# Kernel tuning notes

Hardware: AMD Instinct MI355X
Metric: run time of the kernel (lower is better)

## Reference

```python
import jax, jax.numpy as jnp
import numpy as np

B, S, D = 32, 2048, 1024
TEMP = 9.0  # RelaxedBernoulli temperature (torch.tensor([9]))


def setup_inputs() -> dict:
    key = jax.random.key(0)
    ks = jax.random.split(key, 12)
    sd = 1.0 / np.sqrt(D)
    sd2 = 1.0 / np.sqrt(2 * D)
    return {
        "h_t": jax.random.normal(ks[0], (B, D), jnp.float32),
        "h_s": jax.random.normal(ks[1], (B, S, D), jnp.float32),
        "auxi_hs": jax.random.normal(ks[2], (B, S, D), jnp.float32),
        "noise_u": jax.random.uniform(ks[3], (B, S, 1), jnp.float32),
        # linear_map: Linear(2*dim, 1) with bias
        "Wmap": jax.random.normal(ks[4], (2 * D,), jnp.float32) * sd2,
        "bmap": jax.random.normal(ks[5], (), jnp.float32) * sd2,
        # mlp_h: Linear(dim, dim) + Tanh + Linear(dim, 1)
        "W1": jax.random.normal(ks[6], (D, D), jnp.float32) * sd,
        "b1": jax.random.normal(ks[7], (D,), jnp.float32) * sd,
        "W2": jax.random.normal(ks[8], (D,), jnp.float32) * sd,
        "b2": jax.random.normal(ks[9], (), jnp.float32) * sd,
        # linear_out: Linear(2*dim, dim, bias=False) (attn_type='dot')
        "Wout": jax.random.normal(ks[10], (D, 2 * D), jnp.float32) * sd2,
    }


def reference(h_t, h_s, auxi_hs, noise_u, Wmap, bmap, W1, b1, W2, b2, Wout):
    # h_t: (B, D) one-step query; h_s, auxi_hs: (B, S, D)
    d = h_s.shape[-1]
    # linear_map(concat(auxi_hs, H_t)) without materializing the (B,S,2D) concat
    Wm_a, Wm_t = Wmap[:d], Wmap[d:]
    logits_p = jnp.einsum('bsd,d->bs', auxi_hs, Wm_a) + (h_t @ Wm_t)[:, None] + bmap  # (B,S)
    logits_p = logits_p[..., None]  # (B,S,1); note logit(sigmoid(x)) == x
    # RelaxedBernoulli(temp=9, probs=sigmoid(logits_p)).sample() with explicit uniform noise
    eps = 1e-7
    u = jnp.clip(noise_u, eps, 1.0 - eps)
    logistic = jnp.log(u) - jnp.log1p(-u)  # (B,S,1)
    G = jax.nn.sigmoid((logits_p + logistic) / TEMP)  # (B,S,1)
    # mlp_h(h_s): Linear -> tanh -> Linear
    e = jnp.einsum('bsd,d->bs', jnp.tanh(jnp.einsum('bsd,ed->bse', h_s, W1) + b1), W2) + b2
    e = e[..., None]  # (B,S,1)
    # custom softmax: max over dim 0 (batch!), exp, gate
    v = jnp.max(e, axis=0, keepdims=True)  # (1,S,1)
    scores = jnp.exp(e - v) * G  # (B,S,1)
    align = scores[..., 0] / jnp.sum(scores[..., 0], axis=1, keepdims=True)  # (B,S)
    c = jnp.einsum('bs,bsd->bd', align, h_s)  # (B,D)
    attn_h = jnp.tanh(jnp.concatenate([c, h_t], axis=-1) @ Wout.T)  # (B,D)
    return attn_h, align
```

## Files before the change

### kernel.cpp

```cpp
#include <hip/hip_runtime.h>
#include <hip/hip_bf16.h>
#include <math.h>

#define B_ 32
#define S_ 2048
#define D_ 1024
#define TEMP_ 9.0f

typedef __attribute__((ext_vector_type(8))) short short8;
typedef __attribute__((ext_vector_type(4))) float f32x4;
typedef __attribute__((ext_vector_type(4))) unsigned short ushort4v;

__device__ __forceinline__ unsigned short f2b(float f) {
  union { float f; unsigned int u; } v; v.f = f;
  unsigned int r = v.u;
  r += 0x7fffu + ((r >> 16) & 1u);
  return (unsigned short)(r >> 16);
}
__device__ __forceinline__ float b2f(unsigned short b) {
  union { float f; unsigned int u; } v; v.u = ((unsigned int)b) << 16;
  return v.f;
}
__device__ __forceinline__ float tanh_fast(float x) {
  float ez = __expf(2.f * x);
  return 1.f - __fdividef(2.f, ez + 1.f);
}

#define GLOAD_LDS16(g, l) \
  __builtin_amdgcn_global_load_lds((const __attribute__((address_space(1))) void*)(g), \
                                   (__attribute__((address_space(3))) void*)(l), 16, 0, 0)

__global__ void k_conv(const float* __restrict__ src, unsigned short* __restrict__ dst, int n8) {
  int i = blockIdx.x * 256 + threadIdx.x;
  if (i >= n8) return;
  const float4* g = reinterpret_cast<const float4*>(src) + (size_t)i * 2;
  float4 x0 = g[0], x1 = g[1];
  uint4 w;
  w.x = f2b(x0.x) | ((unsigned)f2b(x0.y) << 16);
  w.y = f2b(x0.z) | ((unsigned)f2b(x0.w) << 16);
  w.z = f2b(x1.x) | ((unsigned)f2b(x1.y) << 16);
  w.w = f2b(x1.z) | ((unsigned)f2b(x1.w) << 16);
  reinterpret_cast<uint4*>(dst)[i] = w;
}

__global__ void k0_tdot(const float* __restrict__ h_t, const float* __restrict__ Wmap,
                        const float* __restrict__ bmap, float* __restrict__ tdot) {
  int b = blockIdx.x;
  int t = threadIdx.x;
  float p = 0.f;
  for (int k = t; k < D_; k += 256) p += h_t[b*D_ + k] * Wmap[D_ + k];
  __shared__ float red[256];
  red[t] = p; __syncthreads();
  for (int off = 128; off > 0; off >>= 1) { if (t < off) red[t] += red[t+off]; __syncthreads(); }
  if (t == 0) tdot[b] = red[0] + bmap[0];
}

__global__ void k1_gate(const float* __restrict__ aux, const float* __restrict__ Wmap,
                        const float* __restrict__ noise, const float* __restrict__ tdot,
                        float* __restrict__ Gout) {
  int w = (blockIdx.x * 256 + threadIdx.x) >> 6;
  int lane = threadIdx.x & 63;
  const float4* arow = reinterpret_cast<const float4*>(aux + (size_t)w * D_);
  const float4* wrow = reinterpret_cast<const float4*>(Wmap);
  float p = 0.f;
  for (int it = 0; it < 4; ++it) {
    float4 a = arow[it*64 + lane];
    float4 m = wrow[it*64 + lane];
    p += a.x*m.x + a.y*m.y + a.z*m.z + a.w*m.w;
  }
  for (int msk = 32; msk > 0; msk >>= 1) p += __shfl_xor(p, msk);
  if (lane == 0) {
    int b = w >> 11;
    float logits = p + tdot[b];
    float u = noise[w];
    u = fminf(fmaxf(u, 1e-7f), 1.f - 1e-7f);
    float logistic = logf(u) - log1pf(-u);
    float x = (logits + logistic) / TEMP_;
    Gout[w] = 1.f / (1.f + expf(-x));
  }
}

#define BK3 32
#define NT3 (D_ / BK3)
#define A_BYTES 8192
#define B_BYTES 16384
#define BUF_BYTES 24576
#define NBUF 3

extern __shared__ unsigned short lds2[];

__global__ __launch_bounds__(256, 2) void k2_pipe(
    const unsigned short* __restrict__ Ag, const unsigned short* __restrict__ Bg,
    const float* __restrict__ b1, const float* __restrict__ W2,
    float* __restrict__ e_buf) {
  int hw = blockIdx.x;
  int xcd = hw & 7;
  int sub = hw >> 3;
  int cc  = sub & 3;
  int rc  = xcd + 8 * (sub >> 2);
  int rowBase = rc * 128;
  int colBase = cc * 256;

  int t = threadIdx.x;
  int lane = t & 63;
  int wc = t >> 6;
  int kslot = lane >> 4;

  int aOff[8], bOff[4];
#pragma unroll
  for (int m = 0; m < 8; ++m) {
    int ra = m * 16 + (lane & 15);
    aOff[m] = ra * 64 + ((kslot ^ ((ra >> 1) & 3)) << 4);
  }
#pragma unroll
  for (int n = 0; n < 4; ++n) {
    int rb = wc * 64 + n * 16 + (lane & 15);
    bOff[n] = A_BYTES + rb * 64 + ((kslot ^ ((rb >> 1) & 3)) << 4);
  }

  const unsigned short* gA[2];
  const unsigned short* gB[4];
  int dstA[2], dstB[4];
#pragma unroll
  for (int i = 0; i < 2; ++i) {
    int c = i * 256 + t;
    int r = c >> 2;
    int clog = (c & 3) ^ ((r >> 1) & 3);
    gA[i] = Ag + (size_t)(rowBase + r) * D_ + clog * 8;
    dstA[i] = c * 16;
  }
#pragma unroll
  for (int i = 0; i < 4; ++i) {
    int c = i * 256 + t;
    int r = c >> 2;
    int clog = (c & 3) ^ ((r >> 1) & 3);
    gB[i] = Bg + (size_t)(colBase + r) * D_ + clog * 8;
    dstB[i] = A_BYTES + c * 16;
  }

  f32x4 acc[8][4] = {};

#define STAGE(TT) do {                                                         \
    char* _ba = (char*)lds2 + ((TT) % NBUF) * BUF_BYTES;                       \
    GLOAD_LDS16(gA[0] + (TT) * 32, _ba + dstA[0]);                             \
    GLOAD_LDS16(gA[1] + (TT) * 32, _ba + dstA[1]);                             \
    GLOAD_LDS16(gB[0] + (TT) * 32, _ba + dstB[0]);                             \
    GLOAD_LDS16(gB[1] + (TT) * 32, _ba + dstB[1]);                             \
    GLOAD_LDS16(gB[2] + (TT) * 32, _ba + dstB[2]);                             \
    GLOAD_LDS16(gB[3] + (TT) * 32, _ba + dstB[3]);                             \
  } while (0)

#define K2_TILE(T, VM, DO_STAGE) do {                                          \
    asm volatile("s_waitcnt lgkmcnt(0)\n\ts_waitcnt vmcnt(" #VM ")" ::: "memory"); \
    __builtin_amdgcn_s_barrier();                                              \
    const char* _ab = (const char*)lds2 + ((T) % NBUF) * BUF_BYTES;            \
    short8 af[8], bf[4];                                                       \
    _Pragma("unroll")                                                          \
    for (int n = 0; n < 4; ++n)                                                \
      bf[n] = *reinterpret_cast<const short8*>(_ab + bOff[n]);                 \
    _Pragma("unroll")                                                          \
    for (int m = 0; m < 4; ++m)                                                \
      af[m] = *reinterpret_cast<const short8*>(_ab + aOff[m]);                 \
    if (DO_STAGE) STAGE((T) + 2);                                              \
    __builtin_amdgcn_s_setprio(1);                                             \
    _Pragma("unroll")                                                          \
    for (int m = 0; m < 4; ++m)                                                \
      _Pragma("unroll")                                                        \
      for (int n = 0; n < 4; ++n)                                              \
        acc[m][n] = __builtin_amdgcn_mfma_f32_16x16x32_bf16(af[m], bf[n], acc[m][n], 0, 0, 0); \
    __builtin_amdgcn_s_setprio(0);                                             \
    _Pragma("unroll")                                                          \
    for (int m = 4; m < 8; ++m)                                                \
      af[m] = *reinterpret_cast<const short8*>(_ab + aOff[m]);                 \
    __builtin_amdgcn_s_setprio(1);                                             \
    _Pragma("unroll")                                                          \
    for (int m = 4; m < 8; ++m)                                                \
      _Pragma("unroll")                                                        \
      for (int n = 0; n < 4; ++n)                                              \
        acc[m][n] = __builtin_amdgcn_mfma_f32_16x16x32_bf16(af[m], bf[n], acc[m][n], 0, 0, 0); \
    __builtin_amdgcn_s_setprio(0);                                             \
  } while (0)

  STAGE(0); STAGE(1);
#pragma unroll
  for (int tt = 0; tt < 30; ++tt) K2_TILE(tt, 6, true);
  K2_TILE(30, 6, false);
  K2_TILE(31, 0, false);
#undef K2_TILE
#undef STAGE

  float b1v[4], w2v[4];
#pragma unroll
  for (int n = 0; n < 4; ++n) {
    int col = colBase + wc * 64 + n * 16 + (lane & 15);
    b1v[n] = b1[col];
    w2v[n] = W2[col];
  }
#pragma unroll
  for (int m = 0; m < 8; ++m) {
#pragma unroll
    for (int j = 0; j < 4; ++j) {
      float s = 0.f;
#pragma unroll
      for (int n = 0; n < 4; ++n)
        s += tanh_fast(acc[m][n][j] + b1v[n]) * w2v[n];
      s += __shfl_xor(s, 1);
      s += __shfl_xor(s, 2);
      s += __shfl_xor(s, 4);
      s += __shfl_xor(s, 8);
      if ((lane & 15) == 0) {
        int row = rowBase + m * 16 + ((lane >> 4) << 2) + j;
        atomicAdd(&e_buf[row], s);
      }
    }
  }
}

#define BM 128
#define BN 128
#define BK 64
__global__ __launch_bounds__(256) void k2_egemm_f32(
    const float* __restrict__ h_s, const float* __restrict__ W1,
    const float* __restrict__ b1, const float* __restrict__ W2,
    float* __restrict__ e_buf) {
  __shared__ unsigned short As[BM * BK];
  __shared__ unsigned short Bs[BN * BK];
  int bid = blockIdx.x;
  int colBase = (bid & 7) * BN;
  int rowBase = (bid >> 3) * BM;
  int t = threadIdx.x;
  int lane = t & 63;
  int wave = t >> 6;
  int wr = wave >> 1, wc = wave & 1;
  f32x4 acc[4][4] = {};
  for (int k0 = 0; k0 < D_; k0 += BK) {
    __syncthreads();
    for (int i = 0; i < 4; ++i) {
      int flat = i*256 + t;
      int r = flat >> 3;
      int c8 = flat & 7;
      int byte = (r*128 + c8*16) ^ ((r & 7) << 4);
      {
        const float4* g = reinterpret_cast<const float4*>(h_s + (size_t)(rowBase + r)*D_ + k0 + c8*8);
        float4 x0 = g[0], x1 = g[1];
        uint4 w;
        w.x = f2b(x0.x) | ((unsigned)f2b(x0.y) << 16);
        w.y = f2b(x0.z) | ((unsigned)f2b(x0.w) << 16);
        w.z = f2b(x1.x) | ((unsigned)f2b(x1.y) << 16);
        w.w = f2b(x1.z) | ((unsigned)f2b(x1.w) << 16);
        *reinterpret_cast<uint4*>(reinterpret_cast<char*>(As) + byte) = w;
      }
      {
        const float4* g = reinterpret_cast<const float4*>(W1 + (size_t)(colBase + r)*D_ + k0 + c8*8);
        float4 x0 = g[0], x1 = g[1];
        uint4 w;
        w.x = f2b(x0.x) | ((unsigned)f2b(x0.y) << 16);
        w.y = f2b(x0.z) | ((unsigned)f2b(x0.w) << 16);
        w.z = f2b(x1.x) | ((unsigned)f2b(x1.y) << 16);
        w.w = f2b(x1.z) | ((unsigned)f2b(x1.w) << 16);
        *reinterpret_cast<uint4*>(reinterpret_cast<char*>(Bs) + byte) = w;
      }
    }
    __syncthreads();
    for (int kk = 0; kk < BK; kk += 32) {
      short8 af[4], bf[4];
      int kByte = kk*2 + ((lane >> 4) << 4);
      for (int m = 0; m < 4; ++m) {
        int r = wr*64 + m*16 + (lane & 15);
        int byte = (r*128 + kByte) ^ ((r & 7) << 4);
        af[m] = *reinterpret_cast<const short8*>(reinterpret_cast<const char*>(As) + byte);
      }
      for (int n = 0; n < 4; ++n) {
        int r = wc*64 + n*16 + (lane & 15);
        int byte = (r*128 + kByte) ^ ((r & 7) << 4);
        bf[n] = *reinterpret_cast<const short8*>(reinterpret_cast<const char*>(Bs) + byte);
      }
      for (int m = 0; m < 4; ++m)
        for (int n = 0; n < 4; ++n)
          acc[m][n] = __builtin_amdgcn_mfma_f32_16x16x32_bf16(af[m], bf[n], acc[m][n], 0, 0, 0);
    }
  }
  float b1v[4], w2v[4];
  for (int n = 0; n < 4; ++n) {
    int col = colBase + wc*64 + n*16 + (lane & 15);
    b1v[n] = b1[col];
    w2v[n] = W2[col];
  }
  for (int m = 0; m < 4; ++m) {
    for (int j = 0; j < 4; ++j) {
      float s = 0.f;
      for (int n = 0; n < 4; ++n)
        s += tanhf(acc[m][n][j] + b1v[n]) * w2v[n];
      s += __shfl_xor(s, 1);
      s += __shfl_xor(s, 2);
      s += __shfl_xor(s, 4);
      s += __shfl_xor(s, 8);
      if ((lane & 15) == 0) {
        int row = rowBase + wr*64 + m*16 + ((lane >> 4) << 2) + j;
        atomicAdd(&e_buf[row], s);
      }
    }
  }
}

__global__ void k3a_vmax(const float* __restrict__ e_buf, float* __restrict__ v) {
  int s = blockIdx.x * 256 + threadIdx.x;
  if (s >= S_) return;
  float m = -1e30f;
  for (int b = 0; b < B_; ++b) m = fmaxf(m, e_buf[b*S_ + s]);
  v[s] = m;
}

__global__ void k3b_align(const float* __restrict__ e_buf, const float* __restrict__ v,
                          float* __restrict__ galign) {
  int b = blockIdx.x;
  int t = threadIdx.x;
  __shared__ float sc[S_];
  __shared__ float red[256];
  float p = 0.f;
  for (int s = t; s < S_; s += 256) {
    float x = expf(e_buf[b*S_ + s] - v[s]) * galign[b*S_ + s];
    sc[s] = x;
    p += x;
  }
  red[t] = p; __syncthreads();
  for (int off = 128; off > 0; off >>= 1) { if (t < off) red[t] += red[t+off]; __syncthreads(); }
  float inv = 1.f / red[0];
  for (int s = t; s < S_; s += 256) galign[b*S_ + s] = sc[s] * inv;
}

__global__ void k4_ctx_bf16(const unsigned short* __restrict__ hsb, const float* __restrict__ align,
                            float* __restrict__ c) {
  int bid = blockIdx.x;
  int b = bid >> 6;
  int sBase = (bid & 63) * 32;
  int t = threadIdx.x;
  float4 accv = {0.f, 0.f, 0.f, 0.f};
  for (int si = 0; si < 32; ++si) {
    int s = sBase + si;
    float a = align[b*S_ + s];
    ushort4v hv = *reinterpret_cast<const ushort4v*>(hsb + (size_t)(b*S_ + s)*D_ + t*4);
    accv.x += a*b2f(hv.x); accv.y += a*b2f(hv.y); accv.z += a*b2f(hv.z); accv.w += a*b2f(hv.w);
  }
  atomicAdd(&c[b*D_ + t*4 + 0], accv.x);
  atomicAdd(&c[b*D_ + t*4 + 1], accv.y);
  atomicAdd(&c[b*D_ + t*4 + 2], accv.z);
  atomicAdd(&c[b*D_ + t*4 + 3], accv.w);
}

__global__ void k4_ctx_f32(const float* __restrict__ h_s, const float* __restrict__ align,
                           float* __restrict__ c) {
  int bid = blockIdx.x;
  int b = bid >> 6;
  int sBase = (bid & 63) * 32;
  int t = threadIdx.x;
  float4 accv = {0.f, 0.f, 0.f, 0.f};
  for (int si = 0; si < 32; ++si) {
    int s = sBase + si;
    float a = align[b*S_ + s];
    float4 hv = *reinterpret_cast<const float4*>(h_s + (size_t)(b*S_ + s)*D_ + t*4);
    accv.x += a*hv.x; accv.y += a*hv.y; accv.z += a*hv.z; accv.w += a*hv.w;
  }
  atomicAdd(&c[b*D_ + t*4 + 0], accv.x);
  atomicAdd(&c[b*D_ + t*4 + 1], accv.y);
  atomicAdd(&c[b*D_ + t*4 + 2], accv.z);
  atomicAdd(&c[b*D_ + t*4 + 3], accv.w);
}

__global__ void k5_out(const float* __restrict__ c, const float* __restrict__ h_t,
                       const float* __restrict__ Wout, float* __restrict__ out) {
  int W = (blockIdx.x * 256 + threadIdx.x) >> 6;
  int lane = threadIdx.x & 63;
  int b = W >> 10;
  int o = W & 1023;
  const float* wrow = Wout + (size_t)o * (2 * D_);
  float p = 0.f;
  for (int it = 0; it < 16; ++it) {
    int k = it*64 + lane;
    p += c[b*D_ + k] * wrow[k];
  }
  for (int it = 16; it < 32; ++it) {
    int k = it*64 + lane;
    p += h_t[b*D_ + (k - D_)] * wrow[k];
  }
  for (int m = 32; m > 0; m >>= 1) p += __shfl_xor(p, m);
  if (lane == 0) out[b*D_ + o] = tanhf(p);
}

extern "C" void kernel_launch(void* const* d_in, const int* in_sizes, int n_in,
                              void* d_out, int out_size, void* d_ws, size_t ws_size,
                              hipStream_t stream) {
  const float* h_t   = (const float*)d_in[0];
  const float* h_s   = (const float*)d_in[1];
  const float* aux   = (const float*)d_in[2];
  const float* noise = (const float*)d_in[3];
  const float* Wmap  = (const float*)d_in[4];
  const float* bmap  = (const float*)d_in[5];
  const float* W1    = (const float*)d_in[6];
  const float* b1    = (const float*)d_in[7];
  const float* W2    = (const float*)d_in[8];
  const float* Wout  = (const float*)d_in[10];

  float* out    = (float*)d_out;
  float* galign = out + B_*D_;

  const size_t HS_N   = (size_t)B_*S_*D_;
  const size_t W1_N   = (size_t)D_*D_;
  const size_t needed = HS_N*2 + W1_N*2 + (65536 + 32 + 2048 + 32768) * sizeof(float);

  if (ws_size >= needed) {
    unsigned short* hs_bf = (unsigned short*)d_ws;
    unsigned short* w1_bf = hs_bf + HS_N;
    float* fws   = (float*)(w1_bf + W1_N);
    float* e_buf = fws;
    float* tdot  = fws + 65536;
    float* v     = fws + 65568;
    float* c     = fws + 67616;

    hipMemsetAsync(e_buf, 0, 65536 * sizeof(float), stream);
    hipMemsetAsync(c, 0, 32768 * sizeof(float), stream);

    hipFuncSetAttribute(reinterpret_cast<const void*>(k2_pipe),
                        hipFuncAttributeMaxDynamicSharedMemorySize, NBUF * BUF_BYTES);

    k_conv<<<(int)(HS_N/8/256), 256, 0, stream>>>(h_s, hs_bf, (int)(HS_N/8));
    k_conv<<<(int)(W1_N/8/256), 256, 0, stream>>>(W1, w1_bf, (int)(W1_N/8));
    k0_tdot<<<32, 256, 0, stream>>>(h_t, Wmap, bmap, tdot);
    k1_gate<<<16384, 256, 0, stream>>>(aux, Wmap, noise, tdot, galign);
    k2_pipe<<<2048, 256, NBUF * BUF_BYTES, stream>>>(hs_bf, w1_bf, b1, W2, e_buf);
    k3a_vmax<<<8, 256, 0, stream>>>(e_buf, v);
    k3b_align<<<32, 256, 0, stream>>>(e_buf, v, galign);
    k4_ctx_bf16<<<2048, 256, 0, stream>>>(hs_bf, galign, c);
    k5_out<<<8192, 256, 0, stream>>>(c, h_t, Wout, out);
  } else {
    float* ws    = (float*)d_ws;
    float* e_buf = ws;
    float* tdot  = ws + 65536;
    float* v     = ws + 65568;
    float* c     = ws + 67616;

    hipMemsetAsync(e_buf, 0, 65536 * sizeof(float), stream);
    hipMemsetAsync(c, 0, 32768 * sizeof(float), stream);

    k0_tdot<<<32, 256, 0, stream>>>(h_t, Wmap, bmap, tdot);
    k1_gate<<<16384, 256, 0, stream>>>(aux, Wmap, noise, tdot, galign);
    k2_egemm_f32<<<4096, 256, 0, stream>>>(h_s, W1, b1, W2, e_buf);
    k3a_vmax<<<8, 256, 0, stream>>>(e_buf, v);
    k3b_align<<<32, 256, 0, stream>>>(e_buf, v, galign);
    k4_ctx_f32<<<2048, 256, 0, stream>>>(h_s, galign, c);
    k5_out<<<8192, 256, 0, stream>>>(c, h_t, Wout, out);
  }
}
```

Measured before the change: 357.2 us.

## Pre-pack W1 into MFMA fragment layout and load B operand directly into registers

A new kernel packs W1 into bf16 in MFMA B-fragment order, so each wave can read its B operands straight from global memory into registers, double-buffered across K tiles. Only the A tile now goes through LDS, with a 4-deep ring of 8KB buffers staged three tiles ahead. The aim is to cut LDS traffic, barrier pressure and LDS footprint in the main GEMM. The cost is that B reads no longer share data within a block: each wave issues its own global loads, which makes the loop more exposed to global memory latency.

```diff
diff --git a/kernel.cpp b/kernel.cpp
--- a/kernel.cpp
+++ b/kernel.cpp
@@ -41,6 +41,24 @@
   w.z = f2b(x1.x) | ((unsigned)f2b(x1.y) << 16);
   w.w = f2b(x1.z) | ((unsigned)f2b(x1.w) << 16);
   reinterpret_cast<uint4*>(dst)[i] = w;
+}
+
+__global__ void k_pack_w1(const float* __restrict__ W1, unsigned short* __restrict__ w1t) {
+  int c = blockIdx.x * 256 + threadIdx.x;
+  int l  = c & 63;
+  int kt = (c >> 6) & 31;
+  int cg = c >> 11;
+  int col = cg * 16 + (l & 15);
+  int k0  = kt * 32 + (l >> 4) * 8;
+  const float* src = W1 + (size_t)col * D_ + k0;
+  float4 x0 = *reinterpret_cast<const float4*>(src);
+  float4 x1 = *reinterpret_cast<const float4*>(src + 4);
+  uint4 w;
+  w.x = f2b(x0.x) | ((unsigned)f2b(x0.y) << 16);
+  w.y = f2b(x0.z) | ((unsigned)f2b(x0.w) << 16);
+  w.z = f2b(x1.x) | ((unsigned)f2b(x1.y) << 16);
+  w.w = f2b(x1.z) | ((unsigned)f2b(x1.w) << 16);
+  reinterpret_cast<uint4*>(w1t)[c] = w;
 }
 
 __global__ void k0_tdot(const float* __restrict__ h_t, const float* __restrict__ Wmap,
@@ -80,17 +98,12 @@
   }
 }
 
-#define BK3 32
-#define NT3 (D_ / BK3)
-#define A_BYTES 8192
-#define B_BYTES 16384
-#define BUF_BYTES 24576
-#define NBUF 3
+#define NT3 32
 
 extern __shared__ unsigned short lds2[];
 
-__global__ __launch_bounds__(256, 2) void k2_pipe(
-    const unsigned short* __restrict__ Ag, const unsigned short* __restrict__ Bg,
+__global__ __launch_bounds__(256, 2) void k2_breg(
+    const unsigned short* __restrict__ Ag, const unsigned short* __restrict__ w1t,
     const float* __restrict__ b1, const float* __restrict__ W2,
     float* __restrict__ e_buf) {
   int hw = blockIdx.x;
@@ -103,24 +116,18 @@
 
   int t = threadIdx.x;
   int lane = t & 63;
-  int wc = t >> 6;
+  int wv = t >> 6;
   int kslot = lane >> 4;
 
-  int aOff[8], bOff[4];
+  int aOff[8];
 #pragma unroll
   for (int m = 0; m < 8; ++m) {
-    int ra = m * 16 + (lane & 15);
-    aOff[m] = ra * 64 + ((kslot ^ ((ra >> 1) & 3)) << 4);
-  }
-#pragma unroll
-  for (int n = 0; n < 4; ++n) {
-    int rb = wc * 64 + n * 16 + (lane & 15);
-    bOff[n] = A_BYTES + rb * 64 + ((kslot ^ ((rb >> 1) & 3)) << 4);
+    int r = m * 16 + (lane & 15);
+    aOff[m] = r * 64 + ((kslot ^ ((r >> 1) & 3)) << 4);
   }
 
   const unsigned short* gA[2];
-  const unsigned short* gB[4];
-  int dstA[2], dstB[4];
+  int dstA[2];
 #pragma unroll
   for (int i = 0; i < 2; ++i) {
     int c = i * 256 + t;
@@ -129,70 +136,69 @@
     gA[i] = Ag + (size_t)(rowBase + r) * D_ + clog * 8;
     dstA[i] = c * 16;
   }
-#pragma unroll
-  for (int i = 0; i < 4; ++i) {
-    int c = i * 256 + t;
-    int r = c >> 2;
-    int clog = (c & 3) ^ ((r >> 1) & 3);
-    gB[i] = Bg + (size_t)(colBase + r) * D_ + clog * 8;
-    dstB[i] = A_BYTES + c * 16;
+
+  const unsigned short* pB[4];
+#pragma unroll
+  for (int n = 0; n < 4; ++n) {
+    int cg = (colBase >> 4) + wv * 4 + n;
+    pB[n] = w1t + (size_t)cg * 16384 + lane * 8;
   }
 
   f32x4 acc[8][4] = {};
+  short8 bfA[4], bfB[4];
 
 #define STAGE(TT) do {                                                         \
-    char* _ba = (char*)lds2 + ((TT) % NBUF) * BUF_BYTES;                       \
+    char* _ba = (char*)lds2 + ((TT) & 3) * 8192;                               \
     GLOAD_LDS16(gA[0] + (TT) * 32, _ba + dstA[0]);                             \
     GLOAD_LDS16(gA[1] + (TT) * 32, _ba + dstA[1]);                             \
-    GLOAD_LDS16(gB[0] + (TT) * 32, _ba + dstB[0]);                             \
-    GLOAD_LDS16(gB[1] + (TT) * 32, _ba + dstB[1]);                             \
-    GLOAD_LDS16(gB[2] + (TT) * 32, _ba + dstB[2]);                             \
-    GLOAD_LDS16(gB[3] + (TT) * 32, _ba + dstB[3]);                             \
   } while (0)
 
-#define K2_TILE(T, VM, DO_STAGE) do {                                          \
+#define K2_TILE(T, VM, DO_B, DO_S, BFC, BFN) do {                              \
     asm volatile("s_waitcnt lgkmcnt(0)\n\ts_waitcnt vmcnt(" #VM ")" ::: "memory"); \
     __builtin_amdgcn_s_barrier();                                              \
-    const char* _ab = (const char*)lds2 + ((T) % NBUF) * BUF_BYTES;            \
-    short8 af[8], bf[4];                                                       \
+    const char* _ab = (const char*)lds2 + ((T) & 3) * 8192;                    \
+    short8 af[8];                                                              \
     _Pragma("unroll")                                                          \
-    for (int n = 0; n < 4; ++n)                                                \
-      bf[n] = *reinterpret_cast<const short8*>(_ab + bOff[n]);                 \
-    _Pragma("unroll")                                                          \
-    for (int m = 0; m < 4; ++m)                                                \
+    for (int m = 0; m < 8; ++m)                                                \
       af[m] = *reinterpret_cast<const short8*>(_ab + aOff[m]);                 \
-    if (DO_STAGE) STAGE((T) + 2);                                              \
+    if (DO_B) {                                                                \
+      _Pragma("unroll")                                                        \
+      for (int n = 0; n < 4; ++n)                                              \
+        BFN[n] = *reinterpret_cast<const short8*>(pB[n] + ((T) + 1) * 512);    \
+    }                                                                          \
+    if (DO_S) STAGE((T) + 3);                                                  \
     __builtin_amdgcn_s_setprio(1);                                             \
     _Pragma("unroll")                                                          \
-    for (int m = 0; m < 4; ++m)                                                \
+    for (int m = 0; m < 8; ++m)                                                \
       _Pragma("unroll")                                                        \
       for (int n = 0; n < 4; ++n)                                              \
-        acc[m][n] = __builtin_amdgcn_mfma_f32_16x16x32_bf16(af[m], bf[n], acc[m][n], 0, 0, 0); \
-    __builtin_amdgcn_s_setprio(0);                                             \
-    _Pragma("unroll")                                                          \
-    for (int m = 4; m < 8; ++m)                                                \
-      af[m] = *reinterpret_cast<const short8*>(_ab + aOff[m]);                 \
-    __builtin_amdgcn_s_setprio(1);                                             \
-    _Pragma("unroll")                                                          \
-    for (int m = 4; m < 8; ++m)                                                \
-      _Pragma("unroll")                                                        \
-      for (int n = 0; n < 4; ++n)                                              \
-        acc[m][n] = __builtin_amdgcn_mfma_f32_16x16x32_bf16(af[m], bf[n], acc[m][n], 0, 0, 0); \
+        acc[m][n] = __builtin_amdgcn_mfma_f32_16x16x32_bf16(af[m], BFC[n], acc[m][n], 0, 0, 0); \
     __builtin_amdgcn_s_setprio(0);                                             \
   } while (0)
 
-  STAGE(0); STAGE(1);
-#pragma unroll
-  for (int tt = 0; tt < 30; ++tt) K2_TILE(tt, 6, true);
-  K2_TILE(30, 6, false);
-  K2_TILE(31, 0, false);
+  STAGE(0); STAGE(1); STAGE(2);
+#pragma unroll
+  for (int n = 0; n < 4; ++n)
+    bfA[n] = *reinterpret_cast<const short8*>(pB[n]);
+
+  K2_TILE(0, 0, true, true, bfA, bfB);
+  K2_TILE(1, 2, true, true, bfB, bfA);
+#pragma unroll
+  for (int tt = 2; tt < 28; tt += 2) {
+    K2_TILE(tt,     2, true, true, bfA, bfB);
+    K2_TILE(tt + 1, 2, true, true, bfB, bfA);
+  }
+  K2_TILE(28, 2, true,  true,  bfA, bfB);
+  K2_TILE(29, 2, true,  false, bfB, bfA);
+  K2_TILE(30, 0, true,  false, bfA, bfB);
+  K2_TILE(31, 0, false, false, bfB, bfA);
 #undef K2_TILE
 #undef STAGE
 
   float b1v[4], w2v[4];
 #pragma unroll
   for (int n = 0; n < 4; ++n) {
-    int col = colBase + wc * 64 + n * 16 + (lane & 15);
+    int col = colBase + wv * 64 + n * 16 + (lane & 15);
     b1v[n] = b1[col];
     w2v[n] = W2[col];
   }
@@ -410,8 +416,8 @@
 
   if (ws_size >= needed) {
     unsigned short* hs_bf = (unsigned short*)d_ws;
-    unsigned short* w1_bf = hs_bf + HS_N;
-    float* fws   = (float*)(w1_bf + W1_N);
+    unsigned short* w1t   = hs_bf + HS_N;
+    float* fws   = (float*)(w1t + W1_N);
     float* e_buf = fws;
     float* tdot  = fws + 65536;
     float* v     = fws + 65568;
@@ -420,14 +426,14 @@
     hipMemsetAsync(e_buf, 0, 65536 * sizeof(float), stream);
     hipMemsetAsync(c, 0, 32768 * sizeof(float), stream);
 
-    hipFuncSetAttribute(reinterpret_cast<const void*>(k2_pipe),
-                        hipFuncAttributeMaxDynamicSharedMemorySize, NBUF * BUF_BYTES);
+    hipFuncSetAttribute(reinterpret_cast<const void*>(k2_breg),
+                        hipFuncAttributeMaxDynamicSharedMemorySize, 32768);
 
     k_conv<<<(int)(HS_N/8/256), 256, 0, stream>>>(h_s, hs_bf, (int)(HS_N/8));
-    k_conv<<<(int)(W1_N/8/256), 256, 0, stream>>>(W1, w1_bf, (int)(W1_N/8));
+    k_pack_w1<<<512, 256, 0, stream>>>(W1, w1t);
     k0_tdot<<<32, 256, 0, stream>>>(h_t, Wmap, bmap, tdot);
     k1_gate<<<16384, 256, 0, stream>>>(aux, Wmap, noise, tdot, galign);
-    k2_pipe<<<2048, 256, NBUF * BUF_BYTES, stream>>>(hs_bf, w1_bf, b1, W2, e_buf);
+    k2_breg<<<2048, 256, 32768, stream>>>(hs_bf, w1t, b1, W2, e_buf);
     k3a_vmax<<<8, 256, 0, stream>>>(e_buf, v);
     k3b_align<<<32, 256, 0, stream>>>(e_buf, v, galign);
     k4_ctx_bf16<<<2048, 256, 0, stream>>>(hs_bf, galign, c);
```

Result: no change. 353.3 us (-1.1%).
